# Kernel tuning notes

Hardware: AMD Instinct MI355X
Metric: run time of the kernel (lower is better)

The kernel has to match this reference:

```python
import jax, jax.numpy as jnp
import numpy as np

B = 4096
OBS, ACT, RDIM = 128, 32, 4
HID = 1024                      # embedding output / head hidden dim
DIMS = [OBS + ACT + RDIM, 128, 128, RDIM]   # target net: 164 -> 128 -> 128 -> 4
N_LAYERS = len(DIMS) - 1


def setup_inputs() -> dict:
    key = jax.random.key(0)
    ks = iter(jax.random.split(key, 64))

    def p(shape, scale=0.02):
        return jax.random.normal(next(ks), shape, jnp.float32) * scale

    inp = {
        "obs": jax.random.normal(next(ks), (B, OBS), jnp.float32),
        "action": jax.random.normal(next(ks), (B, ACT), jnp.float32),
        "prefs": jax.random.uniform(next(ks), (B, RDIM), jnp.float32),
        # embedding MLP (hypernet): (obs, prefs) -> z
        "We1": p((OBS + RDIM, HID)), "be1": jnp.zeros((HID,), jnp.float32),
        "We2": p((HID, HID)), "be2": jnp.zeros((HID,), jnp.float32),
    }
    # head nets: per target layer, linear heads emitting weight / bias / scale
    for i in range(N_LAYERS):
        din, dout = DIMS[i], DIMS[i + 1]
        inp[f"Ww{i}"] = p((HID, dout * din))
        inp[f"bw{i}"] = jnp.zeros((dout * din,), jnp.float32)
        inp[f"Wb{i}"] = p((HID, dout))
        inp[f"bb{i}"] = jnp.zeros((dout,), jnp.float32)
        inp[f"Ws{i}"] = p((HID, dout))
        inp[f"bs{i}"] = jnp.ones((dout,), jnp.float32)  # scale ~ 1 at init
    return inp


def reference(obs, action, prefs, We1, be1, We2, be2,
              Ww0, bw0, Wb0, bb0, Ws0, bs0,
              Ww1, bw1, Wb1, bb1, Ws1, bs1,
              Ww2, bw2, Wb2, bb2, Ws2, bs2):
    # hypernet embedding z  (hypernet_inputs = [obs, prefs])
    hin = jnp.concatenate([obs, prefs], axis=-1)          # [B, 132]
    z = jax.nn.relu(hin @ We1 + be1)
    z = jax.nn.relu(z @ We2 + be2)                        # [B, HID]

    heads = [(Ww0, bw0, Wb0, bb0, Ws0, bs0),
             (Ww1, bw1, Wb1, bb1, Ws1, bs1),
             (Ww2, bw2, Wb2, bb2, Ws2, bs2)]

    # target network input (target_net_inputs = [obs, action, prefs])
    x = jnp.concatenate([obs, action, prefs], axis=-1)    # [B, 164]

    for i, (Ww, bw, Wb, bb, Ws, bs) in enumerate(heads):
        din, dout = DIMS[i], DIMS[i + 1]
        w = (z @ Ww + bw).reshape(-1, dout, din)          # per-sample [B, dout, din]
        b = z @ Wb + bb                                   # [B, dout]
        s = z @ Ws + bs                                   # [B, dout]
        x = (jnp.einsum('bi,boi->bo', x, w) + b) * s      # batched matmul+bias+scale
        if i < N_LAYERS - 1:                              # activation_mask: all but last
            x = jax.nn.relu(x)
    return x                                              # [B, reward_dim]
```

## Files before the change

### kernel.cpp

```cpp
#include <hip/hip_runtime.h>
#include <hip/hip_bf16.h>
#include <stdint.h>

#define B4 4096
#define KZ 1088
#define KH 160

typedef short bf16x8 __attribute__((ext_vector_type(8)));
typedef float f32x4 __attribute__((ext_vector_type(4)));

__device__ __forceinline__ float b2f(uint16_t u){
  union {float f; uint32_t i;} v; v.i = ((uint32_t)u)<<16; return v.f;
}
__device__ __forceinline__ uint16_t f2b(float f){
  union {float fv; uint32_t i;} v; v.fv = f;
  uint32_t r = v.i + 0x7FFFu + ((v.i>>16)&1u);
  return (uint16_t)(r>>16);
}
__device__ __forceinline__ void gload16(const void* g, void* l){
  __builtin_amdgcn_global_load_lds(
      (__attribute__((address_space(1))) void*)(g),
      (__attribute__((address_space(3))) void*)(l), 16, 0, 0);
}

__global__ __launch_bounds__(256) void transpose_pack(
    const float* __restrict__ src, const float* __restrict__ bias,
    uint16_t* __restrict__ dst,
    int Ncols, int Kdst, int Ksrc, int src_ld, int din_dst, int din_src)
{
  __shared__ float tile[32][33];
  int ct = blockIdx.x, kt = blockIdx.y;
  int tid = threadIdx.x;
  int cl = tid & 31, kg = tid >> 5;
  #pragma unroll
  for (int r = 0; r < 4; ++r){
    int kl = kg*4 + r;
    int k  = kt*32 + kl;
    int c  = ct*32 + cl;
    float v = 0.f;
    if (c < Ncols){
      int o = c / din_dst, i = c - o*din_dst;
      if (i < din_src){
        int sc = o*din_src + i;
        if (k < Ksrc)       v = src[(size_t)k*src_ld + sc];
        else if (k == Ksrc) v = bias[sc];
      }
    }
    tile[kl][cl] = v;
  }
  __syncthreads();
  int c_loc = tid >> 3, kq = tid & 7;
  int c = ct*32 + c_loc;
  if (c < Ncols){
    ushort4 st;
    uint16_t* sp = (uint16_t*)&st;
    #pragma unroll
    for (int r = 0; r < 4; ++r) sp[r] = f2b(tile[kq*4 + r][c_loc]);
    *(ushort4*)&dst[(size_t)c*Kdst + kt*32 + kq*4] = st;
  }
}

__global__ __launch_bounds__(256) void pack_hin(
    const float* __restrict__ obs, const float* __restrict__ prefs,
    uint16_t* __restrict__ hinp)
{
  int idx = blockIdx.x*256 + threadIdx.x;
  int b = idx / KH, k = idx - b*KH;
  float v;
  if (k < 128)      v = obs[b*128 + k];
  else if (k < 132) v = prefs[b*4 + (k-128)];
  else              v = (k == 132) ? 1.f : 0.f;
  hinp[idx] = f2b(v);
}

__global__ __launch_bounds__(256) void pack_x0T(
    const float* __restrict__ obs, const float* __restrict__ act,
    const float* __restrict__ prefs, uint16_t* __restrict__ x0T)
{
  int idx = blockIdx.x*256 + threadIdx.x;
  int c = idx >> 12;
  int b = idx & (B4-1);
  float v = 0.f;
  if (c < 128)      v = obs[b*128 + c];
  else if (c < 160) v = act[b*32 + (c-128)];
  else if (c < 164) v = prefs[b*4 + (c-160)];
  x0T[idx] = f2b(v);
}

__global__ __launch_bounds__(256) void zinit(uint16_t* __restrict__ z1p,
                                             uint16_t* __restrict__ zp)
{
  int idx = blockIdx.x*256 + threadIdx.x;
  int t = idx & 127;
  int row = idx >> 7;
  uint16_t* p = (t < 64) ? z1p : zp;
  int col = 1024 + (t & 63);
  p[(size_t)row*KZ + col] = ((t & 63) == 0) ? (uint16_t)0x3F80 : (uint16_t)0;
}

template<int RELU, int OUTBF, int TRANS>
__global__ __launch_bounds__(256) void gemm128(
    const uint16_t* __restrict__ A, int lda,
    const uint16_t* __restrict__ BT, int ldb,
    void* __restrict__ Cv, int ldc, int K)
{
  __shared__ char smA[128*64];
  __shared__ char smB[128*64];
  int tid = threadIdx.x, w = tid >> 6, lane = tid & 63;
  int m0 = blockIdx.x*128, n0 = blockIdx.y*128;
  const uint16_t* Ab = A  + (size_t)m0*lda;
  const uint16_t* Bb = BT + (size_t)n0*ldb;
  f32x4 acc[2][8];
  #pragma unroll
  for (int mf = 0; mf < 2; ++mf)
    #pragma unroll
    for (int nf = 0; nf < 8; ++nf) acc[mf][nf] = (f32x4){0.f,0.f,0.f,0.f};
  int colg = lane & 15, hi = lane >> 4;

  for (int k0 = 0; k0 < K; k0 += 32){
    #pragma unroll
    for (int p = 0; p < 2; ++p){
      int rb = p*4 + w;
      int row = rb*16 + (lane >> 2);
      int chunk = (lane & 3) ^ ((row >> 1) & 3);
      gload16(Ab + (size_t)row*lda + k0 + chunk*8, &smA[rb*1024]);
      gload16(Bb + (size_t)row*ldb + k0 + chunk*8, &smB[rb*1024]);
    }
    __syncthreads();
    bf16x8 af[2];
    #pragma unroll
    for (int mf = 0; mf < 2; ++mf){
      int row = w*32 + mf*16 + colg;
      af[mf] = *(const bf16x8*)&smA[row*64 + ((hi ^ ((row>>1)&3)) << 4)];
    }
    #pragma unroll
    for (int nf = 0; nf < 8; ++nf){
      int row = nf*16 + colg;
      bf16x8 bfr = *(const bf16x8*)&smB[row*64 + ((hi ^ ((row>>1)&3)) << 4)];
      acc[0][nf] = __builtin_amdgcn_mfma_f32_16x16x32_bf16(af[0], bfr, acc[0][nf], 0,0,0);
      acc[1][nf] = __builtin_amdgcn_mfma_f32_16x16x32_bf16(af[1], bfr, acc[1][nf], 0,0,0);
    }
    __syncthreads();
  }
  #pragma unroll
  for (int mf = 0; mf < 2; ++mf){
    #pragma unroll
    for (int nf = 0; nf < 8; ++nf){
      int col = n0 + nf*16 + colg;
      #pragma unroll
      for (int r = 0; r < 4; ++r){
        int row = m0 + w*32 + mf*16 + hi*4 + r;
        float v = acc[mf][nf][r];
        if (RELU) v = v > 0.f ? v : 0.f;
        if (TRANS)      ((float*)Cv)[(size_t)col*ldc + row] = v;
        else if (OUTBF) ((uint16_t*)Cv)[(size_t)row*ldc + col] = f2b(v);
        else            ((float*)Cv)[(size_t)row*ldc + col] = v;
      }
    }
  }
}

template<int DINP>
__global__ __launch_bounds__(512, 2) void hyper2n(
    const uint16_t* __restrict__ zp,
    const uint16_t* __restrict__ WpT,
    const uint16_t* __restrict__ xT,
    const float*  __restrict__ bsbT,
    uint16_t* __restrict__ outT,
    int relu)
{
  constexpr int NF     = DINP/32;
  constexpr int BCALLS = DINP/64;
  constexpr int WAITN  = 2 + BCALLS;
  constexpr int HBUF   = 16384 + 2*DINP*64;
  constexpr int NH     = KZ/32;
  __shared__ char sm[3*HBUF];

  int tid = threadIdx.x, w = tid >> 6, lane = tid & 63;
  int wm = w >> 2, wn = w & 3;
  int f = blockIdx.x;
  int xcd = f & 7;
  int j = f >> 3;
  int pair = j >> 1;
  int mt = xcd*2 + (j & 1);
  int m0 = mt*256;
  const uint16_t* Ag = zp  + (size_t)m0*KZ;
  const uint16_t* Bg = WpT + (size_t)pair*(2*DINP)*KZ;
  int colg = lane & 15, hi = lane >> 4;

  f32x4 acc[8][NF];
  #pragma unroll
  for (int mf = 0; mf < 8; ++mf)
    #pragma unroll
    for (int nf = 0; nf < NF; ++nf) acc[mf][nf] = (f32x4){0.f,0.f,0.f,0.f};

  auto SA = [&](int h, int a){
    int row = a*128 + (tid >> 2);
    int ch  = (tid & 3) ^ ((row >> 1) & 3);
    gload16(Ag + (size_t)row*KZ + h*32 + ch*8,
            sm + (h%3)*HBUF + a*8192 + w*1024);
  };
  auto SB = [&](int h, int b){
    int row = b*128 + (tid >> 2);
    int ch  = (tid & 3) ^ ((row >> 1) & 3);
    gload16(Bg + (size_t)row*KZ + h*32 + ch*8,
            sm + (h%3)*HBUF + 16384 + b*8192 + w*1024);
  };

  SA(0,0); SA(0,1);
  #pragma unroll
  for (int b = 0; b < BCALLS; ++b) SB(0,b);
  SA(1,0); SA(1,1);
  #pragma unroll
  for (int b = 0; b < BCALLS; ++b) SB(1,b);

  for (int h = 0; h < NH; ++h){
    const char* base = sm + (h%3)*HBUF;
    if (h == NH-1) asm volatile("s_waitcnt vmcnt(0)" ::: "memory");
    else           asm volatile("s_waitcnt vmcnt(%0)" :: "i"(WAITN) : "memory");
    __builtin_amdgcn_s_barrier();
    if (h + 2 < NH){
      SA(h+2,0); SA(h+2,1);
      #pragma unroll
      for (int b = 0; b < BCALLS; ++b) SB(h+2,b);
    }
    bf16x8 Bf[NF];
    #pragma unroll
    for (int nf = 0; nf < NF; ++nf){
      int rc = wn*(DINP/2) + nf*16 + colg;
      Bf[nf] = *(const bf16x8*)(base + 16384 + rc*64 + ((hi ^ ((rc>>1)&3)) << 4));
    }
    #pragma unroll
    for (int m = 0; m < 8; ++m){
      int row = wm*128 + m*16 + colg;
      bf16x8 a = *(const bf16x8*)(base + row*64 + ((hi ^ ((row>>1)&3)) << 4));
      #pragma unroll
      for (int nf = 0; nf < NF; ++nf)
        acc[m][nf] = __builtin_amdgcn_mfma_f32_16x16x32_bf16(a, Bf[nf], acc[m][nf], 0,0,0);
    }
  }

  __syncthreads();
  float* red = (float*)sm;
  int parity = wn & 1, o_loc = wn >> 1;
  #pragma unroll
  for (int mf = 0; mf < 8; ++mf){
    float p0=0.f, p1=0.f, p2=0.f, p3=0.f;
    int b0 = m0 + wm*128 + mf*16 + hi*4;
    #pragma unroll
    for (int nf = 0; nf < NF; ++nf){
      int il = parity*(DINP/2) + nf*16 + colg;
      ushort4 xv = *(const ushort4*)(xT + (size_t)il*B4 + b0);
      f32x4 a = acc[mf][nf];
      p0 += a[0]*b2f(xv.x); p1 += a[1]*b2f(xv.y);
      p2 += a[2]*b2f(xv.z); p3 += a[3]*b2f(xv.w);
    }
    #pragma unroll
    for (int off = 1; off < 16; off <<= 1){
      p0 += __shfl_xor(p0, off); p1 += __shfl_xor(p1, off);
      p2 += __shfl_xor(p2, off); p3 += __shfl_xor(p3, off);
    }
    if (colg == 0){
      int rloc = wm*128 + mf*16 + hi*4;
      float* rp = red + parity*512 + o_loc*256 + rloc;
      rp[0] = p0; rp[1] = p1; rp[2] = p2; rp[3] = p3;
    }
  }
  __syncthreads();
  {
    int o_l = tid >> 8, row = tid & 255;
    int o = pair*2 + o_l;
    float v = red[o_l*256 + row] + red[512 + o_l*256 + row];
    float bv = bsbT[(size_t)o*B4 + m0 + row];
    float sv = bsbT[(size_t)(128+o)*B4 + m0 + row];
    float val = (v + bv) * sv;
    if (relu) val = val > 0.f ? val : 0.f;
    outT[(size_t)o*B4 + m0 + row] = f2b(val);
  }
}

__global__ __launch_bounds__(256) void finalize_k(
    const float* __restrict__ w2, const uint16_t* __restrict__ x2T,
    const float* __restrict__ bs2, float* __restrict__ out)
{
  int tid = threadIdx.x;
  int o = tid & 3;
  int b = blockIdx.x*64 + (tid >> 2);
  const float* wr = w2 + (size_t)b*512 + o*128;
  float dot = 0.f;
  #pragma unroll
  for (int i = 0; i < 128; i += 4){
    float4 wv = *(const float4*)(wr + i);
    dot += wv.x * b2f(x2T[(size_t)(i+0)*B4 + b]);
    dot += wv.y * b2f(x2T[(size_t)(i+1)*B4 + b]);
    dot += wv.z * b2f(x2T[(size_t)(i+2)*B4 + b]);
    dot += wv.w * b2f(x2T[(size_t)(i+3)*B4 + b]);
  }
  float bv = bs2[(size_t)b*128 + o];
  float sv = bs2[(size_t)b*128 + 4 + o];
  out[b*4 + o] = (dot + bv) * sv;
}

extern "C" void kernel_launch(void* const* d_in, const int* in_sizes, int n_in,
                              void* d_out, int out_size, void* d_ws, size_t ws_size,
                              hipStream_t stream)
{
  const float* obs   = (const float*)d_in[0];
  const float* act   = (const float*)d_in[1];
  const float* prefs = (const float*)d_in[2];
  const float* We1 = (const float*)d_in[3];
  const float* be1 = (const float*)d_in[4];
  const float* We2 = (const float*)d_in[5];
  const float* be2 = (const float*)d_in[6];
  const float* Ww0 = (const float*)d_in[7],  *bw0 = (const float*)d_in[8];
  const float* Wb0 = (const float*)d_in[9],  *bb0 = (const float*)d_in[10];
  const float* Ws0 = (const float*)d_in[11], *bs0i = (const float*)d_in[12];
  const float* Ww1 = (const float*)d_in[13], *bw1 = (const float*)d_in[14];
  const float* Wb1 = (const float*)d_in[15], *bb1 = (const float*)d_in[16];
  const float* Ws1 = (const float*)d_in[17], *bs1i = (const float*)d_in[18];
  const float* Ww2 = (const float*)d_in[19], *bw2 = (const float*)d_in[20];
  const float* Wb2 = (const float*)d_in[21], *bb2 = (const float*)d_in[22];
  const float* Ws2 = (const float*)d_in[23], *bs2i = (const float*)d_in[24];

  char* ws = (char*)d_ws;
  size_t off = 0;
  auto alloc = [&](size_t bytes)->char*{
    char* p = ws + off; off += (bytes + 255) & ~(size_t)255; return p;
  };
  uint16_t* WpT0  = (uint16_t*)alloc((size_t)24576*KZ*2);
  uint16_t* WpT1  = (uint16_t*)alloc((size_t)16384*KZ*2);
  uint16_t* WpT2  = (uint16_t*)alloc((size_t)512*KZ*2);
  uint16_t* We1T  = (uint16_t*)alloc((size_t)1024*KH*2);
  uint16_t* We2T  = (uint16_t*)alloc((size_t)1024*KZ*2);
  uint16_t* Wbs0T = (uint16_t*)alloc((size_t)256*KZ*2);
  uint16_t* Wbs1T = (uint16_t*)alloc((size_t)256*KZ*2);
  uint16_t* Wbs2T = (uint16_t*)alloc((size_t)128*KZ*2);
  uint16_t* hinp  = (uint16_t*)alloc((size_t)B4*KH*2);
  uint16_t* z1p   = (uint16_t*)alloc((size_t)B4*KZ*2);
  uint16_t* zp    = (uint16_t*)alloc((size_t)B4*KZ*2);
  float*    bsb0  = (float*)alloc((size_t)256*B4*4);
  float*    bsb1  = (float*)alloc((size_t)256*B4*4);
  float*    bsb2  = (float*)alloc((size_t)B4*128*4);
  uint16_t* x0T   = (uint16_t*)alloc((size_t)192*B4*2);
  uint16_t* x1T   = (uint16_t*)alloc((size_t)128*B4*2);
  uint16_t* x2T   = (uint16_t*)alloc((size_t)128*B4*2);
  float*    w2    = (float*)alloc((size_t)B4*512*4);
  (void)ws_size; (void)in_sizes; (void)n_in; (void)out_size;

  hipMemsetAsync(Wbs2T, 0, (size_t)128*KZ*2, stream);

  dim3 blk(256);
  auto tg = [](int nc, int kd){ return dim3((nc+31)/32, kd/32); };
  transpose_pack<<<tg(24576,KZ),blk,0,stream>>>(Ww0, bw0, WpT0, 24576, KZ, 1024, 20992, 192, 164);
  transpose_pack<<<tg(16384,KZ),blk,0,stream>>>(Ww1, bw1, WpT1, 16384, KZ, 1024, 16384, 128, 128);
  transpose_pack<<<tg(512,KZ),blk,0,stream>>>(Ww2, bw2, WpT2, 512, KZ, 1024, 512, 128, 128);
  transpose_pack<<<tg(1024,KH),blk,0,stream>>>(We1, be1, We1T, 1024, KH, 132, 1024, 1024, 1024);
  transpose_pack<<<tg(1024,KZ),blk,0,stream>>>(We2, be2, We2T, 1024, KZ, 1024, 1024, 1024, 1024);
  transpose_pack<<<tg(128,KZ),blk,0,stream>>>(Wb0, bb0, Wbs0T,          128, KZ, 1024, 128, 128, 128);
  transpose_pack<<<tg(128,KZ),blk,0,stream>>>(Ws0, bs0i, Wbs0T + 128*KZ,128, KZ, 1024, 128, 128, 128);
  transpose_pack<<<tg(128,KZ),blk,0,stream>>>(Wb1, bb1, Wbs1T,          128, KZ, 1024, 128, 128, 128);
  transpose_pack<<<tg(128,KZ),blk,0,stream>>>(Ws1, bs1i, Wbs1T + 128*KZ,128, KZ, 1024, 128, 128, 128);
  transpose_pack<<<tg(4,KZ),blk,0,stream>>>(Wb2, bb2, Wbs2T,        4, KZ, 1024, 4, 4, 4);
  transpose_pack<<<tg(4,KZ),blk,0,stream>>>(Ws2, bs2i, Wbs2T + 4*KZ,4, KZ, 1024, 4, 4, 4);

  pack_hin<<<dim3(B4*KH/256),blk,0,stream>>>(obs, prefs, hinp);
  pack_x0T<<<dim3(192*B4/256),blk,0,stream>>>(obs, act, prefs, x0T);
  zinit<<<dim3(B4*128/256),blk,0,stream>>>(z1p, zp);

  gemm128<1,1,0><<<dim3(32,8),blk,0,stream>>>(hinp, KH, We1T, KH, z1p, KZ, KH);
  gemm128<1,1,0><<<dim3(32,8),blk,0,stream>>>(z1p, KZ, We2T, KZ, zp, KZ, KZ);
  gemm128<0,0,1><<<dim3(32,4),blk,0,stream>>>(zp, KZ, Wbs0T, KZ, bsb0, B4, KZ);
  gemm128<0,0,0><<<dim3(32,1),blk,0,stream>>>(zp, KZ, Wbs2T, KZ, bsb2, 128, KZ);

  hyper2n<192><<<dim3(1024),dim3(512),0,stream>>>(zp, WpT0, x0T, bsb0, x1T, 1);
  hyper2n<128><<<dim3(1024),dim3(512),0,stream>>>(zp, WpT1, x1T, bsb1, x2T, 1);

  gemm128<0,0,0><<<dim3(32,4),blk,0,stream>>>(zp, KZ, WpT2, KZ, w2, 512, KZ);
  finalize_k<<<dim3(B4/64),blk,0,stream>>>(w2, x2T, bsb2, (float*)d_out);
}
```

Before: 603.2 us.

## Shrink hypernet fused kernel tile to one output per block, 128 rows

The fused per-sample weight-generation kernel is retiled so each block computes a single target output neuron over 128 batch rows instead of two outputs over 256 rows. Accumulator registers drop, occupancy bounds rise to 4 blocks per SM, and the grid grows fourfold. This is meant to improve latency hiding and load balance. The cost is less reuse of each staged z and weight tile, so global and L2 traffic for the z operand goes up.

```diff
diff --git a/kernel.cpp b/kernel.cpp
--- a/kernel.cpp
+++ b/kernel.cpp
@@ -161,7 +161,7 @@
 }
 
 template<int DINP>
-__global__ __launch_bounds__(512, 2) void hyper2n(
+__global__ __launch_bounds__(512, 4) void hyper1n(
     const uint16_t* __restrict__ zp,
     const uint16_t* __restrict__ WpT,
     const uint16_t* __restrict__ xT,
@@ -169,11 +169,10 @@
     uint16_t* __restrict__ outT,
     int relu)
 {
-  constexpr int NF     = DINP/32;
-  constexpr int BCALLS = DINP/64;
-  constexpr int WAITN  = 2 + BCALLS;
-  constexpr int HBUF   = 16384 + 2*DINP*64;
-  constexpr int NH     = KZ/32;
+  constexpr int NF   = DINP/64;
+  constexpr int NWC  = DINP/4;
+  constexpr int HBUF = 8192 + DINP*64;
+  constexpr int NH   = KZ/32;
   __shared__ char sm[3*HBUF];
 
   int tid = threadIdx.x, w = tid >> 6, lane = tid & 63;
@@ -181,58 +180,63 @@
   int f = blockIdx.x;
   int xcd = f & 7;
   int j = f >> 3;
-  int pair = j >> 1;
-  int mt = xcd*2 + (j & 1);
-  int m0 = mt*256;
+  int o = j >> 2;
+  int mt = xcd*4 + (j & 3);
+  int m0 = mt*128;
   const uint16_t* Ag = zp  + (size_t)m0*KZ;
-  const uint16_t* Bg = WpT + (size_t)pair*(2*DINP)*KZ;
+  const uint16_t* Bg = WpT + (size_t)o*DINP*KZ;
   int colg = lane & 15, hi = lane >> 4;
 
-  f32x4 acc[8][NF];
-  #pragma unroll
-  for (int mf = 0; mf < 8; ++mf)
+  f32x4 acc[4][NF];
+  #pragma unroll
+  for (int mf = 0; mf < 4; ++mf)
     #pragma unroll
     for (int nf = 0; nf < NF; ++nf) acc[mf][nf] = (f32x4){0.f,0.f,0.f,0.f};
 
-  auto SA = [&](int h, int a){
-    int row = a*128 + (tid >> 2);
-    int ch  = (tid & 3) ^ ((row >> 1) & 3);
-    gload16(Ag + (size_t)row*KZ + h*32 + ch*8,
-            sm + (h%3)*HBUF + a*8192 + w*1024);
+  auto STAGE = [&](int h){
+    char* base = sm + (h%3)*HBUF;
+    {
+      int row = tid >> 2;
+      int ch  = (tid & 3) ^ ((row >> 1) & 3);
+      gload16(Ag + (size_t)row*KZ + h*32 + ch*8, base + w*1024);
+    }
+    {
+      int row = tid >> 2;
+      int ch  = (tid & 3) ^ ((row >> 1) & 3);
+      gload16(Bg + (size_t)row*KZ + h*32 + ch*8, base + 8192 + w*1024);
+    }
+    if constexpr (DINP == 192){
+      if (tid < 256){
+        int row = 128 + (tid >> 2);
+        int ch  = (tid & 3) ^ ((row >> 1) & 3);
+        gload16(Bg + (size_t)row*KZ + h*32 + ch*8, base + 16384 + w*1024);
+      }
+    }
   };
-  auto SB = [&](int h, int b){
-    int row = b*128 + (tid >> 2);
-    int ch  = (tid & 3) ^ ((row >> 1) & 3);
-    gload16(Bg + (size_t)row*KZ + h*32 + ch*8,
-            sm + (h%3)*HBUF + 16384 + b*8192 + w*1024);
-  };
-
-  SA(0,0); SA(0,1);
-  #pragma unroll
-  for (int b = 0; b < BCALLS; ++b) SB(0,b);
-  SA(1,0); SA(1,1);
-  #pragma unroll
-  for (int b = 0; b < BCALLS; ++b) SB(1,b);
+
+  STAGE(0); STAGE(1);
 
   for (int h = 0; h < NH; ++h){
     const char* base = sm + (h%3)*HBUF;
-    if (h == NH-1) asm volatile("s_waitcnt vmcnt(0)" ::: "memory");
-    else           asm volatile("s_waitcnt vmcnt(%0)" :: "i"(WAITN) : "memory");
+    if (h == NH-1){
+      asm volatile("s_waitcnt vmcnt(0)" ::: "memory");
+    } else if constexpr (DINP == 192){
+      if (w < 4) asm volatile("s_waitcnt vmcnt(3)" ::: "memory");
+      else       asm volatile("s_waitcnt vmcnt(2)" ::: "memory");
+    } else {
+      asm volatile("s_waitcnt vmcnt(2)" ::: "memory");
+    }
     __builtin_amdgcn_s_barrier();
-    if (h + 2 < NH){
-      SA(h+2,0); SA(h+2,1);
-      #pragma unroll
-      for (int b = 0; b < BCALLS; ++b) SB(h+2,b);
-    }
+    if (h + 2 < NH) STAGE(h+2);
     bf16x8 Bf[NF];
     #pragma unroll
     for (int nf = 0; nf < NF; ++nf){
-      int rc = wn*(DINP/2) + nf*16 + colg;
-      Bf[nf] = *(const bf16x8*)(base + 16384 + rc*64 + ((hi ^ ((rc>>1)&3)) << 4));
-    }
-    #pragma unroll
-    for (int m = 0; m < 8; ++m){
-      int row = wm*128 + m*16 + colg;
+      int rc = wn*NWC + nf*16 + colg;
+      Bf[nf] = *(const bf16x8*)(base + 8192 + rc*64 + ((hi ^ ((rc>>1)&3)) << 4));
+    }
+    #pragma unroll
+    for (int m = 0; m < 4; ++m){
+      int row = wm*64 + m*16 + colg;
       bf16x8 a = *(const bf16x8*)(base + row*64 + ((hi ^ ((row>>1)&3)) << 4));
       #pragma unroll
       for (int nf = 0; nf < NF; ++nf)
@@ -242,14 +246,13 @@
 
   __syncthreads();
   float* red = (float*)sm;
-  int parity = wn & 1, o_loc = wn >> 1;
-  #pragma unroll
-  for (int mf = 0; mf < 8; ++mf){
+  #pragma unroll
+  for (int mf = 0; mf < 4; ++mf){
     float p0=0.f, p1=0.f, p2=0.f, p3=0.f;
-    int b0 = m0 + wm*128 + mf*16 + hi*4;
+    int b0 = m0 + wm*64 + mf*16 + hi*4;
     #pragma unroll
     for (int nf = 0; nf < NF; ++nf){
-      int il = parity*(DINP/2) + nf*16 + colg;
+      int il = wn*NWC + nf*16 + colg;
       ushort4 xv = *(const ushort4*)(xT + (size_t)il*B4 + b0);
       f32x4 a = acc[mf][nf];
       p0 += a[0]*b2f(xv.x); p1 += a[1]*b2f(xv.y);
@@ -261,16 +264,15 @@
       p2 += __shfl_xor(p2, off); p3 += __shfl_xor(p3, off);
     }
     if (colg == 0){
-      int rloc = wm*128 + mf*16 + hi*4;
-      float* rp = red + parity*512 + o_loc*256 + rloc;
+      int rloc = wm*64 + mf*16 + hi*4;
+      float* rp = red + wn*128 + rloc;
       rp[0] = p0; rp[1] = p1; rp[2] = p2; rp[3] = p3;
     }
   }
   __syncthreads();
-  {
-    int o_l = tid >> 8, row = tid & 255;
-    int o = pair*2 + o_l;
-    float v = red[o_l*256 + row] + red[512 + o_l*256 + row];
+  if (tid < 128){
+    int row = tid;
+    float v = red[row] + red[128 + row] + red[256 + row] + red[384 + row];
     float bv = bsbT[(size_t)o*B4 + m0 + row];
     float sv = bsbT[(size_t)(128+o)*B4 + m0 + row];
     float val = (v + bv) * sv;
@@ -372,8 +374,8 @@
   gemm128<0,0,1><<<dim3(32,4),blk,0,stream>>>(zp, KZ, Wbs0T, KZ, bsb0, B4, KZ);
   gemm128<0,0,0><<<dim3(32,1),blk,0,stream>>>(zp, KZ, Wbs2T, KZ, bsb2, 128, KZ);
 
-  hyper2n<192><<<dim3(1024),dim3(512),0,stream>>>(zp, WpT0, x0T, bsb0, x1T, 1);
-  hyper2n<128><<<dim3(1024),dim3(512),0,stream>>>(zp, WpT1, x1T, bsb1, x2T, 1);
+  hyper1n<192><<<dim3(4096),dim3(512),0,stream>>>(zp, WpT0, x0T, bsb0, x1T, 1);
+  hyper1n<128><<<dim3(4096),dim3(512),0,stream>>>(zp, WpT1, x1T, bsb1, x2T, 1);
 
   gemm128<0,0,0><<<dim3(32,4),blk,0,stream>>>(zp, KZ, WpT2, KZ, w2, 512, KZ);
   finalize_k<<<dim3(B4/64),blk,0,stream>>>(w2, x2T, bsb2, (float*)d_out);
```

After: 659.4 us. +9.3%, slower.
